# Performance work log

Measured on AMD Instinct MI355X. Metric: run time of the kernel, lower is better.

The kernel has to match this reference:

```python
import jax, jax.numpy as jnp
import numpy as np

H = 32  # hidden size


def _gru_layer(x_seq, W_ih, W_hh, b_ih, b_hh):
    """x_seq: [B, T, in] -> outputs [B, T, H], final h [B, H]. PyTorch gate order (r, z, n)."""
    B = x_seq.shape[0]
    # Precompute input projections for all timesteps: [T, B, 3H]
    xw = jnp.einsum('bti,gi->tbg', x_seq, W_ih) + b_ih
    h0 = jnp.zeros((B, H), dtype=x_seq.dtype)

    def step(h, xw_t):
        gh = h @ W_hh.T + b_hh                       # [B, 3H]
        r = jax.nn.sigmoid(xw_t[:, :H] + gh[:, :H])
        z = jax.nn.sigmoid(xw_t[:, H:2 * H] + gh[:, H:2 * H])
        n = jnp.tanh(xw_t[:, 2 * H:] + r * gh[:, 2 * H:])
        h_new = (1.0 - z) * n + z * h
        return h_new, h_new

    h_last, ys = jax.lax.scan(step, h0, xw)
    return jnp.transpose(ys, (1, 0, 2)), h_last       # [B, T, H], [B, H]


def setup_inputs() -> dict:
    key = jax.random.key(0)
    ks = jax.random.split(key, 11)
    s = 1.0 / np.sqrt(H)  # PyTorch GRU init scale
    return {
        'x': jax.random.normal(ks[0], (4096, 512, 32), dtype=jnp.float32),
        'W_ih0': jax.random.uniform(ks[1], (96, 32), jnp.float32, -s, s),
        'W_hh0': jax.random.uniform(ks[2], (96, 32), jnp.float32, -s, s),
        'b_ih0': jax.random.uniform(ks[3], (96,), jnp.float32, -s, s),
        'b_hh0': jax.random.uniform(ks[4], (96,), jnp.float32, -s, s),
        'W_ih1': jax.random.uniform(ks[5], (96, 32), jnp.float32, -s, s),
        'W_hh1': jax.random.uniform(ks[6], (96, 32), jnp.float32, -s, s),
        'b_ih1': jax.random.uniform(ks[7], (96,), jnp.float32, -s, s),
        'b_hh1': jax.random.uniform(ks[8], (96,), jnp.float32, -s, s),
        'W_proj': jax.random.uniform(ks[9], (16, 32), jnp.float32, -s, s),
        'b_proj': jax.random.uniform(ks[10], (16,), jnp.float32, -s, s),
    }


def reference(x, W_ih0, W_hh0, b_ih0, b_hh0, W_ih1, W_hh1, b_ih1, b_hh1, W_proj, b_proj):
    y0, _ = _gru_layer(x, W_ih0, W_hh0, b_ih0, b_hh0)        # layer 0 full sequence
    _, h_last = _gru_layer(y0, W_ih1, W_hh1, b_ih1, b_hh1)   # layer 1 final hidden
    # dropout is identity in eval mode
    return h_last @ W_proj.T + b_proj                        # [B, 16]
```

## Files before the change

kernel.cpp:

```cpp
#include <hip/hip_runtime.h>

using bf16x8 = __attribute__((ext_vector_type(8))) short;
using short8 = __attribute__((ext_vector_type(8))) short;
using s16x4  = __attribute__((ext_vector_type(4))) short;
using f32x4  = __attribute__((ext_vector_type(4))) float;
using u32x4  = __attribute__((ext_vector_type(4))) unsigned;
using ull    = unsigned long long;

#define T_SEQ 512
#define MFMA(A, B, C) __builtin_amdgcn_mfma_f32_16x16x32_bf16((A), (B), (C), 0, 0, 0)

#define BARRIER()                                            \
    do {                                                     \
        __builtin_amdgcn_sched_barrier(0);                   \
        asm volatile("s_waitcnt lgkmcnt(0)" ::: "memory");   \
        __builtin_amdgcn_s_barrier();                        \
        __builtin_amdgcn_sched_barrier(0);                   \
    } while (0)

static constexpr float NL2E  = -1.44269504f;
static constexpr float N2L2E = -2.88539008f;

__device__ __forceinline__ void split8_tr(f32x4 a, f32x4 b, bf16x8& hi, bf16x8& lo) {
    u32x4 ua = __builtin_bit_cast(u32x4, a);
    u32x4 ub = __builtin_bit_cast(u32x4, b);
    u32x4 m  = {0xffff0000u, 0xffff0000u, 0xffff0000u, 0xffff0000u};
    f32x4 ra = a - __builtin_bit_cast(f32x4, ua & m);
    f32x4 rb = b - __builtin_bit_cast(f32x4, ub & m);
    short8 sa  = __builtin_bit_cast(short8, a);
    short8 sb  = __builtin_bit_cast(short8, b);
    short8 sra = __builtin_bit_cast(short8, ra);
    short8 srb = __builtin_bit_cast(short8, rb);
    hi = __builtin_shufflevector(sa, sb, 1, 3, 5, 7, 9, 11, 13, 15);
    lo = __builtin_shufflevector(sra, srb, 1, 3, 5, 7, 9, 11, 13, 15);
}

__device__ __forceinline__ void split4_tr(f32x4 a, s16x4& hi, s16x4& lo) {
    u32x4 ua = __builtin_bit_cast(u32x4, a);
    u32x4 m  = {0xffff0000u, 0xffff0000u, 0xffff0000u, 0xffff0000u};
    f32x4 ra = a - __builtin_bit_cast(f32x4, ua & m);
    short8 sa  = __builtin_bit_cast(short8, a);
    short8 sra = __builtin_bit_cast(short8, ra);
    hi = __builtin_shufflevector(sa, sa, 1, 3, 5, 7);
    lo = __builtin_shufflevector(sra, sra, 1, 3, 5, 7);
}

__device__ __forceinline__ void gate4(f32x4 aR, f32x4 aZ, f32x4 iN, f32x4 sN,
                                      float (&hf)[4]) {
    float er[4], ez[4];
    #pragma unroll
    for (int j = 0; j < 4; ++j) er[j] = __builtin_amdgcn_exp2f(aR[j] * NL2E);
    #pragma unroll
    for (int j = 0; j < 4; ++j) ez[j] = __builtin_amdgcn_exp2f(aZ[j] * NL2E);
    float gr[4], gz[4];
    #pragma unroll
    for (int j = 0; j < 4; ++j) gr[j] = __builtin_amdgcn_rcpf(1.f + er[j]);
    #pragma unroll
    for (int j = 0; j < 4; ++j) gz[j] = __builtin_amdgcn_rcpf(1.f + ez[j]);
    float en[4];
    #pragma unroll
    for (int j = 0; j < 4; ++j) {
        float u = fmaf(gr[j], sN[j], iN[j]);
        en[j] = __builtin_amdgcn_exp2f(fminf(u * N2L2E, 126.f));
    }
    float qn[4];
    #pragma unroll
    for (int j = 0; j < 4; ++j) qn[j] = __builtin_amdgcn_rcpf(1.f + en[j]);
    #pragma unroll
    for (int j = 0; j < 4; ++j) {
        float nn = fmaf(en[j] * qn[j], -2.f, 1.f);
        hf[j] = fmaf(gz[j], hf[j] - nn, nn);
    }
}

__global__ __launch_bounds__(256, 1)
void gru2_quad(const float* __restrict__ x,
               const float* __restrict__ W_ih0, const float* __restrict__ W_hh0,
               const float* __restrict__ b_ih0, const float* __restrict__ b_hh0,
               const float* __restrict__ W_ih1, const float* __restrict__ W_hh1,
               const float* __restrict__ b_ih1, const float* __restrict__ b_hh1,
               const float* __restrict__ W_proj, const float* __restrict__ b_proj,
               float* __restrict__ out)
{
    const int tid  = threadIdx.x;
    const int wid  = tid >> 6;
    const int L    = wid >> 1;
    const int m    = wid & 1;
    const int lane = tid & 63;
    const int r16  = lane & 15;
    const int q    = lane >> 4;
    const int b0   = blockIdx.x * 16;

    __shared__ ull pubH[2][2][64][2];
    __shared__ ull pubL[2][2][64][2];

    const float* Wx = L ? W_ih1 : W_ih0;
    const float* Wh = L ? W_hh1 : W_hh0;
    const float* bx = L ? b_ih1 : b_ih0;
    const float* bh = L ? b_hh1 : b_hh0;

    bf16x8 WxH[3], WxL[3], WhH[3], WhL[3];
    f32x4 bxf[3], bhf[3];
    #pragma unroll
    for (int g = 0; g < 3; ++g) {
        const int tile = 2 * g + m;
        const float* p1 = Wx + (16 * tile + r16) * 32 + 4 * q;
        split8_tr(*(const f32x4*)p1, *(const f32x4*)(p1 + 16), WxH[g], WxL[g]);
        const float* p2 = Wh + (16 * tile + r16) * 32 + 4 * q;
        split8_tr(*(const f32x4*)p2, *(const f32x4*)(p2 + 16), WhH[g], WhL[g]);
        bxf[g] = *(const f32x4*)(bx + 16 * tile + 4 * q);
        bhf[g] = *(const f32x4*)(bh + 16 * tile + 4 * q);
    }

    float hf[4] = {0.f, 0.f, 0.f, 0.f};
    bf16x8 inh = {}, inl = {};
    const float* xp = x + (size_t)(b0 + r16) * (T_SEQ * 32) + 4 * q;
    f32x4 xA = {}, xB = {};

    if (L == 0) {
        xA = *(const f32x4*)(xp);
        xB = *(const f32x4*)(xp + 16);
        split8_tr(xA, xB, inh, inl);
        xA = *(const f32x4*)(xp + 32);
        xB = *(const f32x4*)(xp + 48);
        f32x4 iR = MFMA(WxH[0], inh, bxf[0]);
        f32x4 iZ = MFMA(WxH[1], inh, bxf[1]);
        f32x4 iN = MFMA(WxH[2], inh, bxf[2]);
        iR = MFMA(WxH[0], inl, iR); iZ = MFMA(WxH[1], inl, iZ); iN = MFMA(WxH[2], inl, iN);
        iR = MFMA(WxL[0], inh, iR); iZ = MFMA(WxL[1], inh, iZ); iN = MFMA(WxL[2], inh, iN);
        gate4(iR + bhf[0], iZ + bhf[1], iN, bhf[2], hf);
        s16x4 hi4, lo4;
        split4_tr(f32x4{hf[0], hf[1], hf[2], hf[3]}, hi4, lo4);
        pubH[0][0][lane][m] = __builtin_bit_cast(ull, hi4);
        pubL[0][0][lane][m] = __builtin_bit_cast(ull, lo4);
    } else {
        if (m == 0) { pubH[1][1][lane][0] = 0; pubH[1][1][lane][1] = 0; }
        else        { pubL[1][1][lane][0] = 0; pubL[1][1][lane][1] = 0; }
    }

    #pragma unroll 1
    for (int t = 1; t < T_SEQ; ++t) {
        BARRIER();
        const int pPrev = (t - 1) & 1;
        const int pCur  = t & 1;
        bf16x8 Sh, Sl;
        if (L == 0) {
            Sh = __builtin_bit_cast(bf16x8, *(const u32x4*)&pubH[0][pPrev][lane][0]);
            Sl = __builtin_bit_cast(bf16x8, *(const u32x4*)&pubL[0][pPrev][lane][0]);
            split8_tr(xA, xB, inh, inl);
            const float* nx = xp + (size_t)((t + 1 < T_SEQ) ? t + 1 : t) * 32;
            xA = *(const f32x4*)(nx);
            xB = *(const f32x4*)(nx + 16);
        } else {
            inh = __builtin_bit_cast(bf16x8, *(const u32x4*)&pubH[0][pPrev][lane][0]);
            inl = __builtin_bit_cast(bf16x8, *(const u32x4*)&pubL[0][pPrev][lane][0]);
            Sh  = __builtin_bit_cast(bf16x8, *(const u32x4*)&pubH[1][pCur][lane][0]);
            Sl  = __builtin_bit_cast(bf16x8, *(const u32x4*)&pubL[1][pCur][lane][0]);
        }

        f32x4 iR = MFMA(WxH[0], inh, bxf[0]);
        f32x4 iZ = MFMA(WxH[1], inh, bxf[1]);
        f32x4 iN = MFMA(WxH[2], inh, bxf[2]);
        iR = MFMA(WxH[0], inl, iR); iZ = MFMA(WxH[1], inl, iZ); iN = MFMA(WxH[2], inl, iN);
        iR = MFMA(WxL[0], inh, iR); iZ = MFMA(WxL[1], inh, iZ); iN = MFMA(WxL[2], inh, iN);
        f32x4 sR = MFMA(WhH[0], Sh, bhf[0]);
        f32x4 sZ = MFMA(WhH[1], Sh, bhf[1]);
        f32x4 sN = MFMA(WhH[2], Sh, bhf[2]);
        sR = MFMA(WhH[0], Sl, sR); sZ = MFMA(WhH[1], Sl, sZ); sN = MFMA(WhH[2], Sl, sN);
        sR = MFMA(WhL[0], Sh, sR); sZ = MFMA(WhL[1], Sh, sZ); sN = MFMA(WhL[2], Sh, sN);

        gate4(sR + iR, sZ + iZ, iN, sN, hf);

        s16x4 hi4, lo4;
        split4_tr(f32x4{hf[0], hf[1], hf[2], hf[3]}, hi4, lo4);
        const int pW = (L == 0) ? pCur : pPrev;
        pubH[L][pW][lane][m] = __builtin_bit_cast(ull, hi4);
        pubL[L][pW][lane][m] = __builtin_bit_cast(ull, lo4);
    }

    __syncthreads();
    if (L == 1) {
        bf16x8 i2h = __builtin_bit_cast(bf16x8, *(const u32x4*)&pubH[0][1][lane][0]);
        bf16x8 i2l = __builtin_bit_cast(bf16x8, *(const u32x4*)&pubL[0][1][lane][0]);
        bf16x8 Sh  = __builtin_bit_cast(bf16x8, *(const u32x4*)&pubH[1][0][lane][0]);
        bf16x8 Sl  = __builtin_bit_cast(bf16x8, *(const u32x4*)&pubL[1][0][lane][0]);
        f32x4 iR = MFMA(WxH[0], i2h, bxf[0]);
        f32x4 iZ = MFMA(WxH[1], i2h, bxf[1]);
        f32x4 iN = MFMA(WxH[2], i2h, bxf[2]);
        iR = MFMA(WxH[0], i2l, iR); iZ = MFMA(WxH[1], i2l, iZ); iN = MFMA(WxH[2], i2l, iN);
        iR = MFMA(WxL[0], i2h, iR); iZ = MFMA(WxL[1], i2h, iZ); iN = MFMA(WxL[2], i2h, iN);
        f32x4 sR = MFMA(WhH[0], Sh, bhf[0]);
        f32x4 sZ = MFMA(WhH[1], Sh, bhf[1]);
        f32x4 sN = MFMA(WhH[2], Sh, bhf[2]);
        sR = MFMA(WhH[0], Sl, sR); sZ = MFMA(WhH[1], Sl, sZ); sN = MFMA(WhH[2], Sl, sN);
        sR = MFMA(WhL[0], Sh, sR); sZ = MFMA(WhL[1], Sh, sZ); sN = MFMA(WhL[2], Sh, sN);
        gate4(sR + iR, sZ + iZ, iN, sN, hf);
        s16x4 hi4, lo4;
        split4_tr(f32x4{hf[0], hf[1], hf[2], hf[3]}, hi4, lo4);
        pubH[1][1][lane][m] = __builtin_bit_cast(ull, hi4);
        pubL[1][1][lane][m] = __builtin_bit_cast(ull, lo4);
    }
    __syncthreads();

    if (wid == 2) {
        bf16x8 Hh = __builtin_bit_cast(bf16x8, *(const u32x4*)&pubH[1][1][lane][0]);
        bf16x8 Hl = __builtin_bit_cast(bf16x8, *(const u32x4*)&pubL[1][1][lane][0]);
        const float* pp = W_proj + r16 * 32 + 4 * q;
        bf16x8 Wph, Wpl;
        split8_tr(*(const f32x4*)pp, *(const f32x4*)(pp + 16), Wph, Wpl);
        f32x4 accp = *(const f32x4*)(b_proj + 4 * q);
        accp = MFMA(Wph, Hh, accp);
        accp = MFMA(Wph, Hl, accp);
        accp = MFMA(Wpl, Hh, accp);
        #pragma unroll
        for (int rg = 0; rg < 4; ++rg)
            out[(b0 + r16) * 16 + 4 * q + rg] = accp[rg];
    }
}

extern "C" void kernel_launch(void* const* d_in, const int* in_sizes, int n_in,
                              void* d_out, int out_size, void* d_ws, size_t ws_size,
                              hipStream_t stream) {
    const float* x      = (const float*)d_in[0];
    const float* W_ih0  = (const float*)d_in[1];
    const float* W_hh0  = (const float*)d_in[2];
    const float* b_ih0  = (const float*)d_in[3];
    const float* b_hh0  = (const float*)d_in[4];
    const float* W_ih1  = (const float*)d_in[5];
    const float* W_hh1  = (const float*)d_in[6];
    const float* b_ih1  = (const float*)d_in[7];
    const float* b_hh1  = (const float*)d_in[8];
    const float* W_proj = (const float*)d_in[9];
    const float* b_proj = (const float*)d_in[10];
    float* out = (float*)d_out;

    const int nb   = in_sizes[0] / (T_SEQ * 32);
    const int grid = nb / 16;

    hipLaunchKernelGGL(gru2_quad, dim3(grid), dim3(256), 0, stream,
                       x, W_ih0, W_hh0, b_ih0, b_hh0,
                       W_ih1, W_hh1, b_ih1, b_hh1, W_proj, b_proj, out);
}
```

Baseline: 298.2 us.

## Keep own hidden half in registers, read only partner half, prefetch x two steps ahead

The shared hidden-state buffers are re-laid out per producing wave ([m][L][phase][lane]). Each wave keeps its own half of h in registers and reads only the partner wave's half from LDS, which cuts LDS traffic on the per-step critical path. Layer 0 now issues the input-projection MFMAs before reading h, converts x one step ahead and loads x two steps ahead, so more independent work can overlap the barrier wait. The price is more live registers and some extra register shuffling to assemble the MFMA operands.

```diff
diff --git a/kernel.cpp b/kernel.cpp
--- a/kernel.cpp
+++ b/kernel.cpp
@@ -43,6 +43,24 @@
     short8 sra = __builtin_bit_cast(short8, ra);
     hi = __builtin_shufflevector(sa, sa, 1, 3, 5, 7);
     lo = __builtin_shufflevector(sra, sra, 1, 3, 5, 7);
+}
+
+__device__ __forceinline__ bf16x8 combine8(ull lo8, ull hi8) {
+    u32x4 v = {(unsigned)lo8, (unsigned)(lo8 >> 32),
+               (unsigned)hi8, (unsigned)(hi8 >> 32)};
+    return __builtin_bit_cast(bf16x8, v);
+}
+__device__ __forceinline__ bf16x8 combine8_sel(ull own, ull other, int m) {
+    return combine8(m ? other : own, m ? own : other);
+}
+
+__device__ __forceinline__ void mfma9(const bf16x8 (&WH)[3], const bf16x8 (&WL)[3],
+                                      bf16x8 inh, bf16x8 inl,
+                                      f32x4 c0, f32x4 c1, f32x4 c2,
+                                      f32x4& a0, f32x4& a1, f32x4& a2) {
+    a0 = MFMA(WH[0], inh, c0); a1 = MFMA(WH[1], inh, c1); a2 = MFMA(WH[2], inh, c2);
+    a0 = MFMA(WH[0], inl, a0); a1 = MFMA(WH[1], inl, a1); a2 = MFMA(WH[2], inl, a2);
+    a0 = MFMA(WL[0], inh, a0); a1 = MFMA(WL[1], inh, a1); a2 = MFMA(WL[2], inh, a2);
 }
 
 __device__ __forceinline__ void gate4(f32x4 aR, f32x4 aZ, f32x4 iN, f32x4 sN,
@@ -91,8 +109,8 @@
     const int q    = lane >> 4;
     const int b0   = blockIdx.x * 16;
 
-    __shared__ ull pubH[2][2][64][2];
-    __shared__ ull pubL[2][2][64][2];
+    __shared__ ull pubH_[2][2][2][64];
+    __shared__ ull pubL_[2][2][2][64];
 
     const float* Wx = L ? W_ih1 : W_ih0;
     const float* Wh = L ? W_hh1 : W_hh0;
@@ -113,29 +131,32 @@
     }
 
     float hf[4] = {0.f, 0.f, 0.f, 0.f};
-    bf16x8 inh = {}, inl = {};
+    ull ownH = 0, ownL = 0;
     const float* xp = x + (size_t)(b0 + r16) * (T_SEQ * 32) + 4 * q;
     f32x4 xA = {}, xB = {};
+    bf16x8 xh_cur = {}, xl_cur = {};
 
     if (L == 0) {
-        xA = *(const f32x4*)(xp);
-        xB = *(const f32x4*)(xp + 16);
-        split8_tr(xA, xB, inh, inl);
+        f32x4 x0A = *(const f32x4*)(xp);
+        f32x4 x0B = *(const f32x4*)(xp + 16);
         xA = *(const f32x4*)(xp + 32);
         xB = *(const f32x4*)(xp + 48);
-        f32x4 iR = MFMA(WxH[0], inh, bxf[0]);
-        f32x4 iZ = MFMA(WxH[1], inh, bxf[1]);
-        f32x4 iN = MFMA(WxH[2], inh, bxf[2]);
-        iR = MFMA(WxH[0], inl, iR); iZ = MFMA(WxH[1], inl, iZ); iN = MFMA(WxH[2], inl, iN);
-        iR = MFMA(WxL[0], inh, iR); iZ = MFMA(WxL[1], inh, iZ); iN = MFMA(WxL[2], inh, iN);
+        split8_tr(x0A, x0B, xh_cur, xl_cur);
+        f32x4 iR, iZ, iN;
+        mfma9(WxH, WxL, xh_cur, xl_cur, bxf[0], bxf[1], bxf[2], iR, iZ, iN);
         gate4(iR + bhf[0], iZ + bhf[1], iN, bhf[2], hf);
         s16x4 hi4, lo4;
         split4_tr(f32x4{hf[0], hf[1], hf[2], hf[3]}, hi4, lo4);
-        pubH[0][0][lane][m] = __builtin_bit_cast(ull, hi4);
-        pubL[0][0][lane][m] = __builtin_bit_cast(ull, lo4);
+        ownH = __builtin_bit_cast(ull, hi4);
+        ownL = __builtin_bit_cast(ull, lo4);
+        pubH_[m][0][0][lane] = ownH;
+        pubL_[m][0][0][lane] = ownL;
+        split8_tr(xA, xB, xh_cur, xl_cur);
+        xA = *(const f32x4*)(xp + 64);
+        xB = *(const f32x4*)(xp + 80);
     } else {
-        if (m == 0) { pubH[1][1][lane][0] = 0; pubH[1][1][lane][1] = 0; }
-        else        { pubL[1][1][lane][0] = 0; pubL[1][1][lane][1] = 0; }
+        pubH_[m][1][1][lane] = 0;
+        pubL_[m][1][1][lane] = 0;
     }
 
     #pragma unroll 1
@@ -143,68 +164,64 @@
         BARRIER();
         const int pPrev = (t - 1) & 1;
         const int pCur  = t & 1;
-        bf16x8 Sh, Sl;
+        f32x4 iR, iZ, iN, sR, sZ, sN;
         if (L == 0) {
-            Sh = __builtin_bit_cast(bf16x8, *(const u32x4*)&pubH[0][pPrev][lane][0]);
-            Sl = __builtin_bit_cast(bf16x8, *(const u32x4*)&pubL[0][pPrev][lane][0]);
-            split8_tr(xA, xB, inh, inl);
-            const float* nx = xp + (size_t)((t + 1 < T_SEQ) ? t + 1 : t) * 32;
-            xA = *(const f32x4*)(nx);
-            xB = *(const f32x4*)(nx + 16);
+            ull oH = pubH_[1 - m][0][pPrev][lane];
+            ull oL = pubL_[1 - m][0][pPrev][lane];
+            mfma9(WxH, WxL, xh_cur, xl_cur, bxf[0], bxf[1], bxf[2], iR, iZ, iN);
+            bf16x8 Sh = combine8_sel(ownH, oH, m);
+            bf16x8 Sl = combine8_sel(ownL, oL, m);
+            mfma9(WhH, WhL, Sh, Sl, bhf[0], bhf[1], bhf[2], sR, sZ, sN);
+            split8_tr(xA, xB, xh_cur, xl_cur);
+            const int tn = (t + 2 < T_SEQ) ? t + 2 : T_SEQ - 1;
+            xA = *(const f32x4*)(xp + (size_t)tn * 32);
+            xB = *(const f32x4*)(xp + (size_t)tn * 32 + 16);
         } else {
-            inh = __builtin_bit_cast(bf16x8, *(const u32x4*)&pubH[0][pPrev][lane][0]);
-            inl = __builtin_bit_cast(bf16x8, *(const u32x4*)&pubL[0][pPrev][lane][0]);
-            Sh  = __builtin_bit_cast(bf16x8, *(const u32x4*)&pubH[1][pCur][lane][0]);
-            Sl  = __builtin_bit_cast(bf16x8, *(const u32x4*)&pubL[1][pCur][lane][0]);
+            ull i0H = pubH_[0][0][pPrev][lane];
+            ull i1H = pubH_[1][0][pPrev][lane];
+            ull i0L = pubL_[0][0][pPrev][lane];
+            ull i1L = pubL_[1][0][pPrev][lane];
+            ull oH  = pubH_[1 - m][1][pCur][lane];
+            ull oL  = pubL_[1 - m][1][pCur][lane];
+            bf16x8 inh = combine8(i0H, i1H);
+            bf16x8 inl = combine8(i0L, i1L);
+            mfma9(WxH, WxL, inh, inl, bxf[0], bxf[1], bxf[2], iR, iZ, iN);
+            bf16x8 Sh = combine8_sel(ownH, oH, m);
+            bf16x8 Sl = combine8_sel(ownL, oL, m);
+            mfma9(WhH, WhL, Sh, Sl, bhf[0], bhf[1], bhf[2], sR, sZ, sN);
         }
-
-        f32x4 iR = MFMA(WxH[0], inh, bxf[0]);
-        f32x4 iZ = MFMA(WxH[1], inh, bxf[1]);
-        f32x4 iN = MFMA(WxH[2], inh, bxf[2]);
-        iR = MFMA(WxH[0], inl, iR); iZ = MFMA(WxH[1], inl, iZ); iN = MFMA(WxH[2], inl, iN);
-        iR = MFMA(WxL[0], inh, iR); iZ = MFMA(WxL[1], inh, iZ); iN = MFMA(WxL[2], inh, iN);
-        f32x4 sR = MFMA(WhH[0], Sh, bhf[0]);
-        f32x4 sZ = MFMA(WhH[1], Sh, bhf[1]);
-        f32x4 sN = MFMA(WhH[2], Sh, bhf[2]);
-        sR = MFMA(WhH[0], Sl, sR); sZ = MFMA(WhH[1], Sl, sZ); sN = MFMA(WhH[2], Sl, sN);
-        sR = MFMA(WhL[0], Sh, sR); sZ = MFMA(WhL[1], Sh, sZ); sN = MFMA(WhL[2], Sh, sN);
 
         gate4(sR + iR, sZ + iZ, iN, sN, hf);
 
         s16x4 hi4, lo4;
         split4_tr(f32x4{hf[0], hf[1], hf[2], hf[3]}, hi4, lo4);
+        ownH = __builtin_bit_cast(ull, hi4);
+        ownL = __builtin_bit_cast(ull, lo4);
         const int pW = (L == 0) ? pCur : pPrev;
-        pubH[L][pW][lane][m] = __builtin_bit_cast(ull, hi4);
-        pubL[L][pW][lane][m] = __builtin_bit_cast(ull, lo4);
+        pubH_[m][L][pW][lane] = ownH;
+        pubL_[m][L][pW][lane] = ownL;
     }
 
     __syncthreads();
     if (L == 1) {
-        bf16x8 i2h = __builtin_bit_cast(bf16x8, *(const u32x4*)&pubH[0][1][lane][0]);
-        bf16x8 i2l = __builtin_bit_cast(bf16x8, *(const u32x4*)&pubL[0][1][lane][0]);
-        bf16x8 Sh  = __builtin_bit_cast(bf16x8, *(const u32x4*)&pubH[1][0][lane][0]);
-        bf16x8 Sl  = __builtin_bit_cast(bf16x8, *(const u32x4*)&pubL[1][0][lane][0]);
-        f32x4 iR = MFMA(WxH[0], i2h, bxf[0]);
-        f32x4 iZ = MFMA(WxH[1], i2h, bxf[1]);
-        f32x4 iN = MFMA(WxH[2], i2h, bxf[2]);
-        iR = MFMA(WxH[0], i2l, iR); iZ = MFMA(WxH[1], i2l, iZ); iN = MFMA(WxH[2], i2l, iN);
-        iR = MFMA(WxL[0], i2h, iR); iZ = MFMA(WxL[1], i2h, iZ); iN = MFMA(WxL[2], i2h, iN);
-        f32x4 sR = MFMA(WhH[0], Sh, bhf[0]);
-        f32x4 sZ = MFMA(WhH[1], Sh, bhf[1]);
-        f32x4 sN = MFMA(WhH[2], Sh, bhf[2]);
-        sR = MFMA(WhH[0], Sl, sR); sZ = MFMA(WhH[1], Sl, sZ); sN = MFMA(WhH[2], Sl, sN);
-        sR = MFMA(WhL[0], Sh, sR); sZ = MFMA(WhL[1], Sh, sZ); sN = MFMA(WhL[2], Sh, sN);
+        bf16x8 inh = combine8(pubH_[0][0][1][lane], pubH_[1][0][1][lane]);
+        bf16x8 inl = combine8(pubL_[0][0][1][lane], pubL_[1][0][1][lane]);
+        bf16x8 Sh  = combine8_sel(ownH, pubH_[1 - m][1][0][lane], m);
+        bf16x8 Sl  = combine8_sel(ownL, pubL_[1 - m][1][0][lane], m);
+        f32x4 iR, iZ, iN, sR, sZ, sN;
+        mfma9(WxH, WxL, inh, inl, bxf[0], bxf[1], bxf[2], iR, iZ, iN);
+        mfma9(WhH, WhL, Sh, Sl, bhf[0], bhf[1], bhf[2], sR, sZ, sN);
         gate4(sR + iR, sZ + iZ, iN, sN, hf);
         s16x4 hi4, lo4;
         split4_tr(f32x4{hf[0], hf[1], hf[2], hf[3]}, hi4, lo4);
-        pubH[1][1][lane][m] = __builtin_bit_cast(ull, hi4);
-        pubL[1][1][lane][m] = __builtin_bit_cast(ull, lo4);
+        pubH_[m][1][1][lane] = __builtin_bit_cast(ull, hi4);
+        pubL_[m][1][1][lane] = __builtin_bit_cast(ull, lo4);
     }
     __syncthreads();
 
     if (wid == 2) {
-        bf16x8 Hh = __builtin_bit_cast(bf16x8, *(const u32x4*)&pubH[1][1][lane][0]);
-        bf16x8 Hl = __builtin_bit_cast(bf16x8, *(const u32x4*)&pubL[1][1][lane][0]);
+        bf16x8 Hh = combine8(pubH_[0][1][1][lane], pubH_[1][1][1][lane]);
+        bf16x8 Hl = combine8(pubL_[0][1][1][lane], pubL_[1][1][1][lane]);
         const float* pp = W_proj + r16 * 32 + 4 * q;
         bf16x8 Wph, Wpl;
         split8_tr(*(const f32x4*)pp, *(const f32x4*)(pp + 16), Wph, Wpl);
```

New measurement: 295.6 us. No clear change (-0.9%).
